# Optimization experiments

Hardware: AMD Instinct MI355X
Metric: run time of the kernel (lower is better)

The kernel has to match this reference:

```python
import jax, jax.numpy as jnp
import numpy as np
import math

B, S, E, H = 4, 2048, 1024, 16
D = E // H  # head_dim = 64


def setup_inputs() -> dict:
    key = jax.random.key(0)
    ks = jax.random.split(key, 5)
    scale = 1.0 / math.sqrt(E)
    x = jax.random.normal(ks[0], (B, S, E), dtype=jnp.float32)
    attention_mask = jnp.ones((B, S), dtype=jnp.int32)
    W_qkv = jax.random.normal(ks[1], (E, 3 * E), dtype=jnp.float32) * scale
    b_qkv = jnp.zeros((3 * E,), dtype=jnp.float32)
    W_proj = jax.random.normal(ks[2], (E, E), dtype=jnp.float32) * scale
    b_proj = jnp.zeros((E,), dtype=jnp.float32)
    return {"x": x, "attention_mask": attention_mask, "W_qkv": W_qkv,
            "b_qkv": b_qkv, "W_proj": W_proj, "b_proj": b_proj}


def reference(x, attention_mask, W_qkv, b_qkv, W_proj, b_proj):
    b, s, e = x.shape
    qkv = x @ W_qkv + b_qkv                       # [B,S,3E]
    qkv = qkv.reshape(b, s, 3, H, D)
    qkv = jnp.transpose(qkv, (2, 0, 3, 1, 4))     # [3,B,H,S,D]
    q, k, v = qkv[0], qkv[1], qkv[2]
    scores = jnp.einsum('bhqd,bhkd->bhqk', q, k) / math.sqrt(D)
    causal = jnp.tril(jnp.ones((s, s), dtype=bool))[None, None]  # [1,1,S,S]
    neg_inf = jnp.float32(-jnp.inf)
    scores = jnp.where(causal, scores, neg_inf)
    pad = (attention_mask[:, None, None, :s] != 0)               # [B,1,1,S]
    scores = jnp.where(pad, scores, neg_inf)
    attn = jax.nn.softmax(scores, axis=-1)        # dropout=0.0 (eval mode)
    out = jnp.einsum('bhqk,bhkd->bhqd', attn, v)  # [B,H,S,D]
    out = jnp.transpose(out, (0, 2, 1, 3)).reshape(b, s, e)
    return out @ W_proj + b_proj
```

## Files before the change

### kernel.cpp

```cpp
#include <hip/hip_runtime.h>
#include <hip/hip_bf16.h>
#include <cstdint>
#include <cstddef>

#define B_ 4
#define S_ 2048
#define E_ 1024
#define H_ 16
#define D_ 64
#define NEG_BIG (-1e30f)
#define SC2 0.18033688011112043f

typedef __bf16 bf16x8 __attribute__((ext_vector_type(8)));
typedef __bf16 bf16x4v __attribute__((ext_vector_type(4)));
typedef float f32x4 __attribute__((ext_vector_type(4)));
typedef float f32x16 __attribute__((ext_vector_type(16)));

__device__ __forceinline__ void async_copy16(void* lds, const void* g) {
  __builtin_amdgcn_global_load_lds(
      (const __attribute__((address_space(1))) void*)g,
      (__attribute__((address_space(3))) void*)lds, 16, 0, 0);
}

__device__ __forceinline__ float bfu2f(unsigned short u) {
  unsigned v = ((unsigned)u) << 16;
  float f;
  __builtin_memcpy(&f, &v, 4);
  return f;
}
__device__ __forceinline__ unsigned short f2bfu(float f) {
  __hip_bfloat16 h = __float2bfloat16(f);
  unsigned short u;
  __builtin_memcpy(&u, &h, 2);
  return u;
}
__device__ __forceinline__ unsigned pk2(float a, float b) {
  return (unsigned)f2bfu(a) | ((unsigned)f2bfu(b) << 16);
}

__device__ __forceinline__ void pl32swap(unsigned& a, unsigned& b) {
#if defined(__has_builtin)
#if __has_builtin(__builtin_amdgcn_permlane32_swap)
  typedef int i32x2 __attribute__((ext_vector_type(2)));
  i32x2 r = __builtin_amdgcn_permlane32_swap((int)a, (int)b, false, false);
  a = (unsigned)r[0];
  b = (unsigned)r[1];
  return;
#else
  asm("v_permlane32_swap_b32 %0, %1" : "+v"(a), "+v"(b));
  return;
#endif
#else
  asm("v_permlane32_swap_b32 %0, %1" : "+v"(a), "+v"(b));
#endif
}

__global__ __launch_bounds__(256) void probe_dtype(
    const unsigned short* __restrict__ xr, int* __restrict__ flagp) {
  __shared__ int cnt;
  if (threadIdx.x == 0) cnt = 0;
  __syncthreads();
  int bad = 0;
  for (int i = 0; i < 32; ++i) {
    unsigned short u = xr[(threadIdx.x * 32 + i) * 2];
    int e = (u >> 7) & 0xFF;
    if (e == 0xFF || e >= 0x90 || (e != 0 && e <= 0x60)) bad++;
  }
  atomicAdd(&cnt, bad);
  __syncthreads();
  if (threadIdx.x == 0) {
    flagp[0] = (cnt > 512) ? 0 : 1;
    flagp[1] = 1;
  }
}

__global__ __launch_bounds__(256) void convert_to_f32(
    const void* __restrict__ in, float* __restrict__ out,
    const int* __restrict__ flagp, int n) {
  int i = blockIdx.x * blockDim.x + threadIdx.x;
  if (i >= n) return;
  out[i] = (*flagp == 0) ? ((const float*)in)[i]
                         : bfu2f(((const unsigned short*)in)[i]);
}

__global__ __launch_bounds__(256) void mask_bias(
    const int* __restrict__ am, float* __restrict__ mb,
    int* __restrict__ flagp, int n) {
  int i = blockIdx.x * blockDim.x + threadIdx.x;
  if (i < n) {
    int a = am[i];
    mb[i] = a ? 0.f : NEG_BIG;
    if (a == 0) atomicAnd(flagp + 1, 0);
  }
}

__global__ __launch_bounds__(256) void transpose_conv(
    const void* __restrict__ in, unsigned short* __restrict__ out,
    const int* __restrict__ flagp, int R, int C) {
  __shared__ unsigned short t[32][33];
  const int flag = *flagp;
  const int c0 = blockIdx.x * 32, r0 = blockIdx.y * 32;
  const int lc = threadIdx.x & 31, lr = threadIdx.x >> 5;
  for (int i = 0; i < 4; ++i) {
    int r = lr + i * 8;
    size_t idx = (size_t)(r0 + r) * C + c0 + lc;
    t[r][lc] = (flag == 0) ? f2bfu(((const float*)in)[idx])
                           : ((const unsigned short*)in)[idx];
  }
  __syncthreads();
  for (int i = 0; i < 4; ++i) {
    int r = lr + i * 8;
    out[(size_t)(c0 + r) * R + r0 + lc] = t[lc][r];
  }
}

__global__ __launch_bounds__(256) void gemm_x_w(
    const void* __restrict__ Xin, long long xoff,
    const __hip_bfloat16* __restrict__ Bt,
    const float* __restrict__ bias,
    const int* __restrict__ flagp,
    __hip_bfloat16* __restrict__ C,
    int M, int N, int K) {
  __shared__ __align__(16) __hip_bfloat16 As[128 * 32];
  __shared__ __align__(16) __hip_bfloat16 Bs[128 * 32];
  const int flag = *flagp;
  const int tid = threadIdx.x;
  const int lin = blockIdx.x;
  const int mtiles = M >> 7;
  const int mloc = mtiles >> 3;
  const int msh = 31 - __builtin_clz(mloc);
  const int xcd = lin & 7, idx = lin >> 3;
  const int m0 = (xcd * mloc + (idx & (mloc - 1))) << 7;
  const int n0 = (idx >> msh) << 7;
  const int w = tid >> 6, lane = tid & 63;
  const int wm = (w & 1) * 64, wn = (w >> 1) * 64;
  const int lm = lane & 15, kg = lane >> 4;
  const int e0 = tid * 8, e1 = tid * 8 + 2048;
  const int ra = tid >> 2;
  const int sw = ((tid >> 3) & 3);
  const int ca = ((tid & 3) ^ sw) * 8;

  f32x4 acc[4][4] = {};

  for (int k0 = 0; k0 < K; k0 += 32) {
    uint4 aw0, aw1;
    if (flag == 0) {
      const float* A32 = (const float*)Xin + xoff;
      float4 f0 = *(const float4*)(A32 + (size_t)(m0 + ra) * K + k0 + ca);
      float4 f1 = *(const float4*)(A32 + (size_t)(m0 + ra) * K + k0 + ca + 4);
      float4 f2 = *(const float4*)(A32 + (size_t)(m0 + ra + 64) * K + k0 + ca);
      float4 f3 = *(const float4*)(A32 + (size_t)(m0 + ra + 64) * K + k0 + ca + 4);
      aw0 = make_uint4(pk2(f0.x, f0.y), pk2(f0.z, f0.w), pk2(f1.x, f1.y), pk2(f1.z, f1.w));
      aw1 = make_uint4(pk2(f2.x, f2.y), pk2(f2.z, f2.w), pk2(f3.x, f3.y), pk2(f3.z, f3.w));
    } else {
      const unsigned short* A16 = (const unsigned short*)Xin + xoff;
      aw0 = *(const uint4*)(A16 + (size_t)(m0 + ra) * K + k0 + ca);
      aw1 = *(const uint4*)(A16 + (size_t)(m0 + ra + 64) * K + k0 + ca);
    }
    __syncthreads();
    *(uint4*)(As + e0) = aw0;
    *(uint4*)(As + e1) = aw1;
    for (int c = 0; c < 2; ++c) {
      int o = tid * 16 + c * 4096;
      int row = o >> 6, chp = (o >> 4) & 3;
      int gch = chp ^ ((row >> 1) & 3);
      async_copy16((char*)Bs + o, (const char*)(Bt + (size_t)(n0 + row) * K + k0 + gch * 8));
    }
    __syncthreads();
    bf16x8 af[4], bfrag[4];
    for (int t = 0; t < 4; ++t) {
      int rt = wm + t * 16 + lm;
      int ch = kg ^ ((rt >> 1) & 3);
      af[t] = *(const bf16x8*)(As + rt * 32 + ch * 8);
    }
    for (int t = 0; t < 4; ++t) {
      int rt = wn + t * 16 + lm;
      int ch = kg ^ ((rt >> 1) & 3);
      bfrag[t] = *(const bf16x8*)(Bs + rt * 32 + ch * 8);
    }
    for (int tm = 0; tm < 4; ++tm)
      for (int tn = 0; tn < 4; ++tn)
        acc[tm][tn] = __builtin_amdgcn_mfma_f32_16x16x32_bf16(af[tm], bfrag[tn], acc[tm][tn], 0, 0, 0);
  }

  for (int tn = 0; tn < 4; ++tn) {
    int col = n0 + wn + tn * 16 + lm;
    float bv = bias[col];
    for (int tm = 0; tm < 4; ++tm) {
      int rbase = m0 + wm + tm * 16 + kg * 4;
      for (int r = 0; r < 4; ++r)
        C[(size_t)(rbase + r) * N + col] = __float2bfloat16(acc[tm][tn][r] + bv);
    }
  }
}

__global__ __launch_bounds__(256) void gemm_p_out(
    const __hip_bfloat16* __restrict__ A,
    const __hip_bfloat16* __restrict__ Bt,
    const float* __restrict__ bias,
    const int* __restrict__ flagp,
    void* __restrict__ Cv, long long coff,
    int M, int N, int K) {
  __shared__ __align__(16) __hip_bfloat16 As[128 * 32];
  __shared__ __align__(16) __hip_bfloat16 Bs[128 * 32];
  const int flag = *flagp;
  const int tid = threadIdx.x;
  const int lin = blockIdx.x;
  const int mtiles = M >> 7;
  const int mloc = mtiles >> 3;
  const int msh = 31 - __builtin_clz(mloc);
  const int xcd = lin & 7, idx = lin >> 3;
  const int m0 = (xcd * mloc + (idx & (mloc - 1))) << 7;
  const int n0 = (idx >> msh) << 7;
  const int w = tid >> 6, lane = tid & 63;
  const int wm = (w & 1) * 64, wn = (w >> 1) * 64;
  const int lm = lane & 15, kg = lane >> 4;

  f32x4 acc[4][4] = {};

  for (int k0 = 0; k0 < K; k0 += 32) {
    __syncthreads();
    for (int c = 0; c < 2; ++c) {
      int o = tid * 16 + c * 4096;
      int row = o >> 6, chp = (o >> 4) & 3;
      int gch = chp ^ ((row >> 1) & 3);
      async_copy16((char*)As + o, (const char*)(A + (size_t)(m0 + row) * K + k0 + gch * 8));
      async_copy16((char*)Bs + o, (const char*)(Bt + (size_t)(n0 + row) * K + k0 + gch * 8));
    }
    __syncthreads();
    bf16x8 af[4], bfrag[4];
    for (int t = 0; t < 4; ++t) {
      int rt = wm + t * 16 + lm;
      int ch = kg ^ ((rt >> 1) & 3);
      af[t] = *(const bf16x8*)(As + rt * 32 + ch * 8);
    }
    for (int t = 0; t < 4; ++t) {
      int rt = wn + t * 16 + lm;
      int ch = kg ^ ((rt >> 1) & 3);
      bfrag[t] = *(const bf16x8*)(Bs + rt * 32 + ch * 8);
    }
    for (int tm = 0; tm < 4; ++tm)
      for (int tn = 0; tn < 4; ++tn)
        acc[tm][tn] = __builtin_amdgcn_mfma_f32_16x16x32_bf16(af[tm], bfrag[tn], acc[tm][tn], 0, 0, 0);
  }

  for (int tn = 0; tn < 4; ++tn) {
    int col = n0 + wn + tn * 16 + lm;
    float bv = bias[col];
    for (int tm = 0; tm < 4; ++tm) {
      int rbase = m0 + wm + tm * 16 + kg * 4;
      for (int r = 0; r < 4; ++r) {
        float v = acc[tm][tn][r] + bv;
        size_t idx2 = (size_t)coff + (size_t)(rbase + r) * N + col;
        if (flag == 0) ((float*)Cv)[idx2] = v;
        else           ((unsigned short*)Cv)[idx2] = f2bfu(v);
      }
    }
  }
}

#define VSTR 72
__device__ __forceinline__ void attn_subtile(
    int j0s, int wq_min, int wq_max, int qg, int allones,
    const char* kbyte, const float* mbrow,
    uint4& kc0, uint4& kc1, uint4& kc2, uint4& kc3,
    uint4& kn0, uint4& kn1, uint4& kn2, uint4& kn3,
    const bf16x8* bq, const __hip_bfloat16* VTb, int hi,
    float& mrow, float& plocal, f32x16& o0, f32x16& o1) {
  if (j0s > wq_max) return;
  {
    const int jn = j0s + 32;
    if (jn <= wq_max) {
      const char* kp = kbyte + (size_t)jn * 6144;
      kn0 = *(const uint4*)(kp);
      kn1 = *(const uint4*)(kp + 32);
      kn2 = *(const uint4*)(kp + 64);
      kn3 = *(const uint4*)(kp + 96);
    }
  }
  bf16x8 a0, a1, a2, a3;
  __builtin_memcpy(&a0, &kc0, 16);
  __builtin_memcpy(&a1, &kc1, 16);
  __builtin_memcpy(&a2, &kc2, 16);
  __builtin_memcpy(&a3, &kc3, 16);

  f32x16 sacc = {};
  __builtin_amdgcn_s_setprio(1);
  sacc = __builtin_amdgcn_mfma_f32_32x32x16_bf16(a0, bq[0], sacc, 0, 0, 0);
  sacc = __builtin_amdgcn_mfma_f32_32x32x16_bf16(a1, bq[1], sacc, 0, 0, 0);
  sacc = __builtin_amdgcn_mfma_f32_32x32x16_bf16(a2, bq[2], sacc, 0, 0, 0);
  sacc = __builtin_amdgcn_mfma_f32_32x32x16_bf16(a3, bq[3], sacc, 0, 0, 0);
  __builtin_amdgcn_s_setprio(0);

  float mt = NEG_BIG;
  const bool needc = (j0s + 31 > wq_min);
  if (allones) {
    if (needc) {
      #pragma unroll
      for (int r = 0; r < 16; ++r) {
        int key = j0s + (r & 3) + 8 * (r >> 2) + 4 * hi;
        float v = (key <= qg) ? sacc[r] : NEG_BIG;
        sacc[r] = v;
        mt = fmaxf(mt, v);
      }
    } else {
      #pragma unroll
      for (int r = 0; r < 16; ++r) mt = fmaxf(mt, sacc[r]);
    }
    mt *= SC2;
  } else {
    #pragma unroll
    for (int rr = 0; rr < 4; ++rr) {
      float4 mb4 = *(const float4*)(mbrow + j0s + rr * 8 + hi * 4);
      const float* mp = (const float*)&mb4;
      #pragma unroll
      for (int i = 0; i < 4; ++i) {
        int r = rr * 4 + i;
        int key = j0s + i + 8 * rr + 4 * hi;
        float v = fmaf(sacc[r], SC2, mp[i]);
        if (needc) v = (key <= qg) ? v : NEG_BIG;
        sacc[r] = v;
        mt = fmaxf(mt, v);
      }
    }
  }
  mt = fmaxf(mt, __shfl_xor(mt, 32));

  if (!__all(mt <= mrow + 8.f)) {
    float mn = fmaxf(mrow, mt);
    float a = __builtin_exp2f(mrow - mn);
    plocal *= a;
    #pragma unroll
    for (int r = 0; r < 16; ++r) { o0[r] *= a; o1[r] *= a; }
    mrow = mn;
  }

  const float sfac = allones ? SC2 : 1.0f;
  float psl = 0.f;
  unsigned pk[8];
  #pragma unroll
  for (int r2 = 0; r2 < 8; ++r2) {
    float p0 = __builtin_exp2f(fmaf(sacc[2 * r2],     sfac, -mrow));
    float p1 = __builtin_exp2f(fmaf(sacc[2 * r2 + 1], sfac, -mrow));
    psl += p0 + p1;
    pk[r2] = pk2(p0, p1);
  }
  plocal += psl;

  pl32swap(pk[0], pk[2]);
  pl32swap(pk[1], pk[3]);
  pl32swap(pk[4], pk[6]);
  pl32swap(pk[5], pk[7]);

  __builtin_amdgcn_s_setprio(1);
  #pragma unroll
  for (int ks = 0; ks < 2; ++ks) {
    uint4 t = make_uint4(pk[ks * 4 + 0], pk[ks * 4 + 1],
                         pk[ks * 4 + 2], pk[ks * 4 + 3]);
    bf16x8 bp;
    __builtin_memcpy(&bp, &t, 16);
    bf16x8 av0 = *(const bf16x8*)(VTb + ks * 16);
    bf16x8 av1 = *(const bf16x8*)(VTb + 32 * VSTR + ks * 16);
    o0 = __builtin_amdgcn_mfma_f32_32x32x16_bf16(av0, bp, o0, 0, 0, 0);
    o1 = __builtin_amdgcn_mfma_f32_32x32x16_bf16(av1, bp, o1, 0, 0, 0);
  }
  __builtin_amdgcn_s_setprio(0);
}

__global__ __launch_bounds__(256, 3) void attn_flash(
    const __hip_bfloat16* __restrict__ qkv,
    const float* __restrict__ mbias,
    const int* __restrict__ flags,
    __hip_bfloat16* __restrict__ outp) {
  __shared__ __align__(16) __hip_bfloat16 VT[2][64 * VSTR];

  const int tid = threadIdx.x;
  const int lin = blockIdx.x;
  const int nbh = gridDim.x >> 4;
  const int bhloc = nbh >> 3;
  const int bsh = 31 - __builtin_clz(bhloc);
  const int xcd = lin & 7, idx = lin >> 3;
  const int bh = xcd * bhloc + (idx & (bhloc - 1));
  const int bx = idx >> bsh;
  const int qt = 15 - bx;
  const int b = bh >> 4, h = bh & 15;
  const int q0 = qt * 128;
  const size_t rowbase = (size_t)b * S_;
  const int w = tid >> 6, lane = tid & 63;
  const int l31 = lane & 31, hi = lane >> 5;
  const int qg = q0 + w * 32 + l31;
  const int wq_min = q0 + w * 32, wq_max = wq_min + 31;
  const int allones = flags[1];
  const float* mbrow = mbias + rowbase;

  const char* kbyte = (const char*)(qkv + (rowbase + l31) * 3072 + 1024 + h * 64 + hi * 8);

  bf16x8 bq[4];
  {
    const __hip_bfloat16* qp = qkv + (rowbase + qg) * 3072 + h * 64 + hi * 8;
    bq[0] = *(const bf16x8*)(qp);
    bq[1] = *(const bf16x8*)(qp + 16);
    bq[2] = *(const bf16x8*)(qp + 32);
    bq[3] = *(const bf16x8*)(qp + 48);
  }

  const int jmax = 2 * qt + 1;

  uint4 ka0, ka1, ka2, ka3, kb0, kb1, kb2, kb3;
  ka0 = *(const uint4*)(kbyte);
  ka1 = *(const uint4*)(kbyte + 32);
  ka2 = *(const uint4*)(kbyte + 64);
  ka3 = *(const uint4*)(kbyte + 96);
  {
    const __hip_bfloat16* vp = qkv + (rowbase + lane) * 3072 + 2048 + h * 64 + w * 16;
    uint4 v0 = *(const uint4*)(vp);
    uint4 v1 = *(const uint4*)(vp + 8);
    const __hip_bfloat16* p0 = (const __hip_bfloat16*)&v0;
    const __hip_bfloat16* p1 = (const __hip_bfloat16*)&v1;
    #pragma unroll
    for (int e = 0; e < 8; ++e) {
      VT[0][(w * 16 + e) * VSTR + lane] = p0[e];
      VT[0][(w * 16 + 8 + e) * VSTR + lane] = p1[e];
    }
  }

  float mrow = NEG_BIG, plocal = 0.f;
  f32x16 o0 = {}, o1 = {};
  int buf = 0;

  for (int j = 0; j <= jmax; ++j) {
    __syncthreads();
    const int nbuf = buf ^ 1;
    const int j0 = j * 64;
    const bool pre = (j < jmax);
    uint4 vva, vvb;
    if (pre) {
      const __hip_bfloat16* vp = qkv + (rowbase + j0 + 64 + lane) * 3072 + 2048 + h * 64 + w * 16;
      vva = *(const uint4*)(vp);
      vvb = *(const uint4*)(vp + 8);
    }
    const __hip_bfloat16* vb0 = VT[buf] + l31 * VSTR + hi * 8;

    attn_subtile(j0, wq_min, wq_max, qg, allones, kbyte, mbrow,
                 ka0, ka1, ka2, ka3, kb0, kb1, kb2, kb3,
                 bq, vb0, hi, mrow, plocal, o0, o1);
    attn_subtile(j0 + 32, wq_min, wq_max, qg, allones, kbyte, mbrow,
                 kb0, kb1, kb2, kb3, ka0, ka1, ka2, ka3,
                 bq, vb0 + 32, hi, mrow, plocal, o0, o1);

    if (pre) {
      const __hip_bfloat16* p0 = (const __hip_bfloat16*)&vva;
      const __hip_bfloat16* p1 = (const __hip_bfloat16*)&vvb;
      #pragma unroll
      for (int e = 0; e < 8; ++e) {
        VT[nbuf][(w * 16 + e) * VSTR + lane] = p0[e];
        VT[nbuf][(w * 16 + 8 + e) * VSTR + lane] = p1[e];
      }
    }
    buf = nbuf;
  }

  {
    float l = plocal + __shfl_xor(plocal, 32);
    float linv = (l > 0.f) ? 1.f / l : 0.f;
    __hip_bfloat16* ob = outp + (rowbase + qg) * 1024 + h * 64;
    #pragma unroll
    for (int rr = 0; rr < 4; ++rr) {
      bf16x4v ov;
      ov[0] = (__bf16)(o0[rr * 4 + 0] * linv);
      ov[1] = (__bf16)(o0[rr * 4 + 1] * linv);
      ov[2] = (__bf16)(o0[rr * 4 + 2] * linv);
      ov[3] = (__bf16)(o0[rr * 4 + 3] * linv);
      *(bf16x4v*)(ob + rr * 8 + hi * 4) = ov;
      bf16x4v ow;
      ow[0] = (__bf16)(o1[rr * 4 + 0] * linv);
      ow[1] = (__bf16)(o1[rr * 4 + 1] * linv);
      ow[2] = (__bf16)(o1[rr * 4 + 2] * linv);
      ow[3] = (__bf16)(o1[rr * 4 + 3] * linv);
      *(bf16x4v*)(ob + 32 + rr * 8 + hi * 4) = ow;
    }
  }
}

extern "C" void kernel_launch(void* const* d_in, const int* in_sizes, int n_in,
                              void* d_out, int out_size, void* d_ws, size_t ws_size,
                              hipStream_t stream) {
  const bool merged = (ws_size >= (80ull << 20));
  char* ws = (char*)d_ws;
  int*            flag   = (int*)ws;
  float*          bq     = (float*)(ws + 1024);
  float*          bp     = (float*)(ws + 16384);
  float*          mbias  = (float*)(ws + 32768);
  unsigned short* WqkvTu = (unsigned short*)(ws + 65536);
  unsigned short* WprojTu= (unsigned short*)(ws + 65536 + 6291456);
  char*           big    = ws + 65536 + 8388608;
  __hip_bfloat16* qkv    = (__hip_bfloat16*)big;
  __hip_bfloat16* attno  = (__hip_bfloat16*)(big + (merged ? 50331648u : 12582912u));

  probe_dtype<<<1, 256, 0, stream>>>((const unsigned short*)d_in[0], flag);
  convert_to_f32<<<12, 256, 0, stream>>>(d_in[3], bq, flag, 3072);
  convert_to_f32<<<4, 256, 0, stream>>>(d_in[5], bp, flag, 1024);
  mask_bias<<<(B_ * S_) / 256, 256, 0, stream>>>((const int*)d_in[1], mbias, flag, B_ * S_);
  transpose_conv<<<dim3(96, 32), 256, 0, stream>>>(d_in[2], WqkvTu, flag, 1024, 3072);
  transpose_conv<<<dim3(32, 32), 256, 0, stream>>>(d_in[4], WprojTu, flag, 1024, 1024);

  const int nchunk = merged ? 1 : B_;
  const int bsz = merged ? B_ : 1;
  const int Mc = bsz * S_;
  for (int c = 0; c < nchunk; ++c) {
    long long off = (long long)c * S_ * E_;
    gemm_x_w<<<dim3((Mc / 128) * (3072 / 128)), 256, 0, stream>>>(
        d_in[0], off, (const __hip_bfloat16*)WqkvTu, bq, flag, qkv, Mc, 3072, 1024);
    attn_flash<<<dim3((S_ / 128) * (bsz * H_)), 256, 0, stream>>>(
        qkv, mbias + (size_t)c * S_, flag, attno);
    gemm_p_out<<<dim3((Mc / 128) * (1024 / 128)), 256, 0, stream>>>(
        attno, (const __hip_bfloat16*)WprojTu, bp, flag, d_out, off, Mc, 1024, 1024);
  }
}
```

Before: 322.0 us.

## Pre-convert x to bf16, unify GEMMs with K=64 tiles, shrink attention blocks

Adds a separate kernel that converts x to bf16 ahead of time, so the QKV GEMM can use async global-to-LDS copies for both operands. Both GEMMs now share one kernel that stages K=64 per iteration with an 8-chunk XOR swizzle, halving the barrier count. Attention blocks drop from 128 to 64 query rows with 128 threads (two waves), doubling the grid for better load balance on the causal triangle. The trade-offs are an extra pass over x through memory, and each key/value tile being loaded by twice as many blocks.

```diff
diff --git a/kernel.cpp b/kernel.cpp
--- a/kernel.cpp
+++ b/kernel.cpp
@@ -83,6 +83,24 @@
                          : bfu2f(((const unsigned short*)in)[i]);
 }
 
+__global__ __launch_bounds__(256) void conv_x_bf16(
+    const void* __restrict__ in, long long off,
+    unsigned short* __restrict__ out,
+    const int* __restrict__ flagp, int n8) {
+  int i = blockIdx.x * 256 + threadIdx.x;
+  if (i >= n8) return;
+  if (*flagp == 0) {
+    const float* p = (const float*)in + off + (size_t)i * 8;
+    float4 a = *(const float4*)p;
+    float4 b = *(const float4*)(p + 4);
+    uint4 o = make_uint4(pk2(a.x, a.y), pk2(a.z, a.w), pk2(b.x, b.y), pk2(b.z, b.w));
+    *(uint4*)(out + (size_t)i * 8) = o;
+  } else {
+    const unsigned short* p = (const unsigned short*)in + off + (size_t)i * 8;
+    *(uint4*)(out + (size_t)i * 8) = *(const uint4*)p;
+  }
+}
+
 __global__ __launch_bounds__(256) void mask_bias(
     const int* __restrict__ am, float* __restrict__ mb,
     int* __restrict__ flagp, int n) {
@@ -114,15 +132,15 @@
   }
 }
 
-__global__ __launch_bounds__(256) void gemm_x_w(
-    const void* __restrict__ Xin, long long xoff,
+__global__ __launch_bounds__(256) void gemm_bb(
+    const __hip_bfloat16* __restrict__ A,
     const __hip_bfloat16* __restrict__ Bt,
     const float* __restrict__ bias,
-    const int* __restrict__ flagp,
-    __hip_bfloat16* __restrict__ C,
+    const int* __restrict__ flagp, int outmode,
+    void* __restrict__ Cv, long long coff,
     int M, int N, int K) {
-  __shared__ __align__(16) __hip_bfloat16 As[128 * 32];
-  __shared__ __align__(16) __hip_bfloat16 Bs[128 * 32];
+  __shared__ __align__(16) __hip_bfloat16 As[128 * 64];
+  __shared__ __align__(16) __hip_bfloat16 Bs[128 * 64];
   const int flag = *flagp;
   const int tid = threadIdx.x;
   const int lin = blockIdx.x;
@@ -135,115 +153,41 @@
   const int w = tid >> 6, lane = tid & 63;
   const int wm = (w & 1) * 64, wn = (w >> 1) * 64;
   const int lm = lane & 15, kg = lane >> 4;
-  const int e0 = tid * 8, e1 = tid * 8 + 2048;
-  const int ra = tid >> 2;
-  const int sw = ((tid >> 3) & 3);
-  const int ca = ((tid & 3) ^ sw) * 8;
 
   f32x4 acc[4][4] = {};
 
-  for (int k0 = 0; k0 < K; k0 += 32) {
-    uint4 aw0, aw1;
-    if (flag == 0) {
-      const float* A32 = (const float*)Xin + xoff;
-      float4 f0 = *(const float4*)(A32 + (size_t)(m0 + ra) * K + k0 + ca);
-      float4 f1 = *(const float4*)(A32 + (size_t)(m0 + ra) * K + k0 + ca + 4);
-      float4 f2 = *(const float4*)(A32 + (size_t)(m0 + ra + 64) * K + k0 + ca);
-      float4 f3 = *(const float4*)(A32 + (size_t)(m0 + ra + 64) * K + k0 + ca + 4);
-      aw0 = make_uint4(pk2(f0.x, f0.y), pk2(f0.z, f0.w), pk2(f1.x, f1.y), pk2(f1.z, f1.w));
-      aw1 = make_uint4(pk2(f2.x, f2.y), pk2(f2.z, f2.w), pk2(f3.x, f3.y), pk2(f3.z, f3.w));
-    } else {
-      const unsigned short* A16 = (const unsigned short*)Xin + xoff;
-      aw0 = *(const uint4*)(A16 + (size_t)(m0 + ra) * K + k0 + ca);
-      aw1 = *(const uint4*)(A16 + (size_t)(m0 + ra + 64) * K + k0 + ca);
-    }
+  for (int k0 = 0; k0 < K; k0 += 64) {
     __syncthreads();
-    *(uint4*)(As + e0) = aw0;
-    *(uint4*)(As + e1) = aw1;
-    for (int c = 0; c < 2; ++c) {
+    #pragma unroll
+    for (int c = 0; c < 4; ++c) {
       int o = tid * 16 + c * 4096;
-      int row = o >> 6, chp = (o >> 4) & 3;
-      int gch = chp ^ ((row >> 1) & 3);
-      async_copy16((char*)Bs + o, (const char*)(Bt + (size_t)(n0 + row) * K + k0 + gch * 8));
-    }
-    __syncthreads();
-    bf16x8 af[4], bfrag[4];
-    for (int t = 0; t < 4; ++t) {
-      int rt = wm + t * 16 + lm;
-      int ch = kg ^ ((rt >> 1) & 3);
-      af[t] = *(const bf16x8*)(As + rt * 32 + ch * 8);
-    }
-    for (int t = 0; t < 4; ++t) {
-      int rt = wn + t * 16 + lm;
-      int ch = kg ^ ((rt >> 1) & 3);
-      bfrag[t] = *(const bf16x8*)(Bs + rt * 32 + ch * 8);
-    }
-    for (int tm = 0; tm < 4; ++tm)
-      for (int tn = 0; tn < 4; ++tn)
-        acc[tm][tn] = __builtin_amdgcn_mfma_f32_16x16x32_bf16(af[tm], bfrag[tn], acc[tm][tn], 0, 0, 0);
-  }
-
-  for (int tn = 0; tn < 4; ++tn) {
-    int col = n0 + wn + tn * 16 + lm;
-    float bv = bias[col];
-    for (int tm = 0; tm < 4; ++tm) {
-      int rbase = m0 + wm + tm * 16 + kg * 4;
-      for (int r = 0; r < 4; ++r)
-        C[(size_t)(rbase + r) * N + col] = __float2bfloat16(acc[tm][tn][r] + bv);
-    }
-  }
-}
-
-__global__ __launch_bounds__(256) void gemm_p_out(
-    const __hip_bfloat16* __restrict__ A,
-    const __hip_bfloat16* __restrict__ Bt,
-    const float* __restrict__ bias,
-    const int* __restrict__ flagp,
-    void* __restrict__ Cv, long long coff,
-    int M, int N, int K) {
-  __shared__ __align__(16) __hip_bfloat16 As[128 * 32];
-  __shared__ __align__(16) __hip_bfloat16 Bs[128 * 32];
-  const int flag = *flagp;
-  const int tid = threadIdx.x;
-  const int lin = blockIdx.x;
-  const int mtiles = M >> 7;
-  const int mloc = mtiles >> 3;
-  const int msh = 31 - __builtin_clz(mloc);
-  const int xcd = lin & 7, idx = lin >> 3;
-  const int m0 = (xcd * mloc + (idx & (mloc - 1))) << 7;
-  const int n0 = (idx >> msh) << 7;
-  const int w = tid >> 6, lane = tid & 63;
-  const int wm = (w & 1) * 64, wn = (w >> 1) * 64;
-  const int lm = lane & 15, kg = lane >> 4;
-
-  f32x4 acc[4][4] = {};
-
-  for (int k0 = 0; k0 < K; k0 += 32) {
-    __syncthreads();
-    for (int c = 0; c < 2; ++c) {
-      int o = tid * 16 + c * 4096;
-      int row = o >> 6, chp = (o >> 4) & 3;
-      int gch = chp ^ ((row >> 1) & 3);
+      int row = o >> 7, chp = (o >> 4) & 7;
+      int gch = chp ^ (row & 7);
       async_copy16((char*)As + o, (const char*)(A + (size_t)(m0 + row) * K + k0 + gch * 8));
       async_copy16((char*)Bs + o, (const char*)(Bt + (size_t)(n0 + row) * K + k0 + gch * 8));
     }
     __syncthreads();
-    bf16x8 af[4], bfrag[4];
-    for (int t = 0; t < 4; ++t) {
-      int rt = wm + t * 16 + lm;
-      int ch = kg ^ ((rt >> 1) & 3);
-      af[t] = *(const bf16x8*)(As + rt * 32 + ch * 8);
-    }
-    for (int t = 0; t < 4; ++t) {
-      int rt = wn + t * 16 + lm;
-      int ch = kg ^ ((rt >> 1) & 3);
-      bfrag[t] = *(const bf16x8*)(Bs + rt * 32 + ch * 8);
-    }
-    for (int tm = 0; tm < 4; ++tm)
-      for (int tn = 0; tn < 4; ++tn)
-        acc[tm][tn] = __builtin_amdgcn_mfma_f32_16x16x32_bf16(af[tm], bfrag[tn], acc[tm][tn], 0, 0, 0);
-  }
-
+    #pragma unroll
+    for (int kk = 0; kk < 2; ++kk) {
+      bf16x8 af[4], bff[4];
+      #pragma unroll
+      for (int t = 0; t < 4; ++t) {
+        int rt = wm + t * 16 + lm;
+        int ch = (kk * 4 + kg) ^ (rt & 7);
+        af[t] = *(const bf16x8*)(As + rt * 64 + ch * 8);
+        int rb = wn + t * 16 + lm;
+        int chb = (kk * 4 + kg) ^ (rb & 7);
+        bff[t] = *(const bf16x8*)(Bs + rb * 64 + chb * 8);
+      }
+      #pragma unroll
+      for (int tm = 0; tm < 4; ++tm)
+        #pragma unroll
+        for (int tn = 0; tn < 4; ++tn)
+          acc[tm][tn] = __builtin_amdgcn_mfma_f32_16x16x32_bf16(af[tm], bff[tn], acc[tm][tn], 0, 0, 0);
+    }
+  }
+
+  const bool f32out = (outmode != 0 && flag == 0);
   for (int tn = 0; tn < 4; ++tn) {
     int col = n0 + wn + tn * 16 + lm;
     float bv = bias[col];
@@ -251,9 +195,9 @@
       int rbase = m0 + wm + tm * 16 + kg * 4;
       for (int r = 0; r < 4; ++r) {
         float v = acc[tm][tn][r] + bv;
-        size_t idx2 = (size_t)coff + (size_t)(rbase + r) * N + col;
-        if (flag == 0) ((float*)Cv)[idx2] = v;
-        else           ((unsigned short*)Cv)[idx2] = f2bfu(v);
+        size_t oidx = (size_t)coff + (size_t)(rbase + r) * N + col;
+        if (f32out) ((float*)Cv)[oidx] = v;
+        else        ((unsigned short*)Cv)[oidx] = f2bfu(v);
       }
     }
   }
@@ -367,7 +311,7 @@
   __builtin_amdgcn_s_setprio(0);
 }
 
-__global__ __launch_bounds__(256, 3) void attn_flash(
+__global__ __launch_bounds__(128, 4) void attn_flash(
     const __hip_bfloat16* __restrict__ qkv,
     const float* __restrict__ mbias,
     const int* __restrict__ flags,
@@ -376,15 +320,15 @@
 
   const int tid = threadIdx.x;
   const int lin = blockIdx.x;
-  const int nbh = gridDim.x >> 4;
+  const int nbh = gridDim.x >> 5;
   const int bhloc = nbh >> 3;
   const int bsh = 31 - __builtin_clz(bhloc);
   const int xcd = lin & 7, idx = lin >> 3;
   const int bh = xcd * bhloc + (idx & (bhloc - 1));
   const int bx = idx >> bsh;
-  const int qt = 15 - bx;
+  const int qt = 31 - bx;
   const int b = bh >> 4, h = bh & 15;
-  const int q0 = qt * 128;
+  const int q0 = qt * 64;
   const size_t rowbase = (size_t)b * S_;
   const int w = tid >> 6, lane = tid & 63;
   const int l31 = lane & 31, hi = lane >> 5;
@@ -404,7 +348,7 @@
     bq[3] = *(const bf16x8*)(qp + 48);
   }
 
-  const int jmax = 2 * qt + 1;
+  const int jmax = qt;
 
   uint4 ka0, ka1, ka2, ka3, kb0, kb1, kb2, kb3;
   ka0 = *(const uint4*)(kbyte);
@@ -412,15 +356,21 @@
   ka2 = *(const uint4*)(kbyte + 64);
   ka3 = *(const uint4*)(kbyte + 96);
   {
-    const __hip_bfloat16* vp = qkv + (rowbase + lane) * 3072 + 2048 + h * 64 + w * 16;
+    const __hip_bfloat16* vp = qkv + (rowbase + lane) * 3072 + 2048 + h * 64 + w * 32;
     uint4 v0 = *(const uint4*)(vp);
     uint4 v1 = *(const uint4*)(vp + 8);
+    uint4 v2 = *(const uint4*)(vp + 16);
+    uint4 v3 = *(const uint4*)(vp + 24);
     const __hip_bfloat16* p0 = (const __hip_bfloat16*)&v0;
     const __hip_bfloat16* p1 = (const __hip_bfloat16*)&v1;
+    const __hip_bfloat16* p2 = (const __hip_bfloat16*)&v2;
+    const __hip_bfloat16* p3 = (const __hip_bfloat16*)&v3;
     #pragma unroll
     for (int e = 0; e < 8; ++e) {
-      VT[0][(w * 16 + e) * VSTR + lane] = p0[e];
-      VT[0][(w * 16 + 8 + e) * VSTR + lane] = p1[e];
+      VT[0][(w * 32 + e) * VSTR + lane] = p0[e];
+      VT[0][(w * 32 + 8 + e) * VSTR + lane] = p1[e];
+      VT[0][(w * 32 + 16 + e) * VSTR + lane] = p2[e];
+      VT[0][(w * 32 + 24 + e) * VSTR + lane] = p3[e];
     }
   }
 
@@ -433,11 +383,13 @@
     const int nbuf = buf ^ 1;
     const int j0 = j * 64;
     const bool pre = (j < jmax);
-    uint4 vva, vvb;
+    uint4 vva, vvb, vvc, vvd;
     if (pre) {
-      const __hip_bfloat16* vp = qkv + (rowbase + j0 + 64 + lane) * 3072 + 2048 + h * 64 + w * 16;
+      const __hip_bfloat16* vp = qkv + (rowbase + j0 + 64 + lane) * 3072 + 2048 + h * 64 + w * 32;
       vva = *(const uint4*)(vp);
       vvb = *(const uint4*)(vp + 8);
+      vvc = *(const uint4*)(vp + 16);
+      vvd = *(const uint4*)(vp + 24);
     }
     const __hip_bfloat16* vb0 = VT[buf] + l31 * VSTR + hi * 8;
 
@@ -451,10 +403,14 @@
     if (pre) {
       const __hip_bfloat16* p0 = (const __hip_bfloat16*)&vva;
       const __hip_bfloat16* p1 = (const __hip_bfloat16*)&vvb;
+      const __hip_bfloat16* p2 = (const __hip_bfloat16*)&vvc;
+      const __hip_bfloat16* p3 = (const __hip_bfloat16*)&vvd;
       #pragma unroll
       for (int e = 0; e < 8; ++e) {
-        VT[nbuf][(w * 16 + e) * VSTR + lane] = p0[e];
-        VT[nbuf][(w * 16 + 8 + e) * VSTR + lane] = p1[e];
+        VT[nbuf][(w * 32 + e) * VSTR + lane] = p0[e];
+        VT[nbuf][(w * 32 + 8 + e) * VSTR + lane] = p1[e];
+        VT[nbuf][(w * 32 + 16 + e) * VSTR + lane] = p2[e];
+        VT[nbuf][(w * 32 + 24 + e) * VSTR + lane] = p3[e];
       }
     }
     buf = nbuf;
@@ -495,7 +451,9 @@
   unsigned short* WprojTu= (unsigned short*)(ws + 65536 + 6291456);
   char*           big    = ws + 65536 + 8388608;
   __hip_bfloat16* qkv    = (__hip_bfloat16*)big;
-  __hip_bfloat16* attno  = (__hip_bfloat16*)(big + (merged ? 50331648u : 12582912u));
+  char*           anx    = big + (merged ? 50331648u : 12582912u);
+  __hip_bfloat16* attno  = (__hip_bfloat16*)anx;
+  unsigned short* xbf    = (unsigned short*)anx;
 
   probe_dtype<<<1, 256, 0, stream>>>((const unsigned short*)d_in[0], flag);
   convert_to_f32<<<12, 256, 0, stream>>>(d_in[3], bq, flag, 3072);
@@ -509,11 +467,15 @@
   const int Mc = bsz * S_;
   for (int c = 0; c < nchunk; ++c) {
     long long off = (long long)c * S_ * E_;
-    gemm_x_w<<<dim3((Mc / 128) * (3072 / 128)), 256, 0, stream>>>(
-        d_in[0], off, (const __hip_bfloat16*)WqkvTu, bq, flag, qkv, Mc, 3072, 1024);
-    attn_flash<<<dim3((S_ / 128) * (bsz * H_)), 256, 0, stream>>>(
+    conv_x_bf16<<<dim3((Mc * 1024) / 2048), 256, 0, stream>>>(
+        d_in[0], off, xbf, flag, (Mc * 1024) / 8);
+    gemm_bb<<<dim3((Mc / 128) * (3072 / 128)), 256, 0, stream>>>(
+        (const __hip_bfloat16*)xbf, (const __hip_bfloat16*)WqkvTu, bq, flag, 0,
+        qkv, 0, Mc, 3072, 1024);
+    attn_flash<<<dim3((S_ / 64) * (bsz * H_)), 128, 0, stream>>>(
         qkv, mbias + (size_t)c * S_, flag, attno);
-    gemm_p_out<<<dim3((Mc / 128) * (1024 / 128)), 256, 0, stream>>>(
-        attno, (const __hip_bfloat16*)WprojTu, bp, flag, d_out, off, Mc, 1024, 1024);
-  }
-}
+    gemm_bb<<<dim3((Mc / 128) * (1024 / 128)), 256, 0, stream>>>(
+        attno, (const __hip_bfloat16*)WprojTu, bp, flag, 1,
+        d_out, off, Mc, 1024, 1024);
+  }
+}
```

After: 477.3 us. +48.2%, slower.
